# Kernel optimization log

Measured on AMD Instinct MI355X. Metric: run time of the kernel, lower is better.

The kernel has to match this reference:

```python
import jax, jax.numpy as jnp
import numpy as np

N_NODES = 100000
N_EDGES = 1600000


def setup_inputs() -> dict:
    key = jax.random.key(0)
    ks = jax.random.split(key, 6)
    x = jax.random.normal(ks[0], (N_NODES, 128), dtype=jnp.float32)
    edge_index = jax.random.randint(ks[1], (2, N_EDGES), 0, N_NODES, dtype=jnp.int64)
    # glorot-ish scaled weights
    W0 = jax.random.normal(ks[2], (128, 64), dtype=jnp.float32) * (1.0 / np.sqrt(128))
    W1 = jax.random.normal(ks[3], (64, 64), dtype=jnp.float32) * (1.0 / np.sqrt(64))
    W2 = jax.random.normal(ks[4], (64, 40), dtype=jnp.float32) * (1.0 / np.sqrt(64))
    b0 = jnp.zeros((64,), jnp.float32)
    b1 = jnp.zeros((64,), jnp.float32)
    b2 = jnp.zeros((40,), jnp.float32)
    return {"x": x, "edge_index": edge_index, "W0": W0, "b0": b0,
            "W1": W1, "b1": b1, "W2": W2, "b2": b2}


def _gcn_norm(edge_index, n, dtype):
    # PyG gcn_norm: add self-loops, deg over targets, norm = d^-1/2[src]*d^-1/2[dst]
    loop = jnp.arange(n, dtype=edge_index.dtype)
    src = jnp.concatenate([edge_index[0], loop])
    dst = jnp.concatenate([edge_index[1], loop])
    deg = jax.ops.segment_sum(jnp.ones_like(dst, dtype=dtype), dst, num_segments=n)
    dinv = jnp.where(deg > 0, jax.lax.rsqrt(deg), 0.0)
    return src, dst, dinv[src] * dinv[dst]


def reference(x, edge_index, W0, b0, W1, b1, W2, b2):
    n = x.shape[0]
    src, dst, norm = _gcn_norm(edge_index, n, x.dtype)

    def conv(h, W, b):
        h = h @ W                                   # [N, out]
        msg = h[src] * norm[:, None]                # gather + per-edge scale
        return jax.ops.segment_sum(msg, dst, num_segments=n) + b

    # dropout skipped (eval mode); relu between layers per forward()
    h = jax.nn.relu(conv(x, W0, b0))
    h = jax.nn.relu(conv(h, W1, b1))
    return conv(h, W2, b2)
```

## Files before the change

### kernel.cpp

```cpp
#include <hip/hip_runtime.h>
#include <hip/hip_fp16.h>


#define ALIGN256(x) (((size_t)(x) + 255) & ~(size_t)255)

typedef _Float16 f16;
typedef f16 f16x8 __attribute__((ext_vector_type(8)));
typedef float f32x4 __attribute__((ext_vector_type(4)));


__global__ __launch_bounds__(256) void k_coarse(const int* __restrict__ ei,
                                                int* __restrict__ ccnt,
                                                int E, int NBUK) {
    __shared__ int h[512];
    int t = threadIdx.x;
    for (int i = t; i < NBUK; i += 256) h[i] = 0;
    __syncthreads();
    int e0 = blockIdx.x * 8192;
    int e1 = min(e0 + 8192, E);
    for (int e = e0 + t; e < e1; e += 256) atomicAdd(&h[ei[E + e] >> 8], 1);
    __syncthreads();
    for (int i = t; i < NBUK; i += 256) {
        int c = h[i];
        if (c) atomicAdd(&ccnt[i], c);
    }
}


__global__ __launch_bounds__(256) void k_cscan(const int* __restrict__ ccnt,
                                               int* __restrict__ cbase,
                                               int* __restrict__ cpos,
                                               int* __restrict__ row_start,
                                               int NBUK, int E, int N) {
    __shared__ int sd[256];
    int t = threadIdx.x;
    int i0 = 2 * t, i1 = 2 * t + 1;
    int v0 = (i0 < NBUK) ? ccnt[i0] : 0;
    int v1 = (i1 < NBUK) ? ccnt[i1] : 0;
    int s = v0 + v1;
    sd[t] = s;
    __syncthreads();
    for (int off = 1; off < 256; off <<= 1) {
        int u = (t >= off) ? sd[t - off] : 0;
        __syncthreads();
        sd[t] += u;
        __syncthreads();
    }
    int base = sd[t] - s;
    if (i0 < NBUK) { cbase[i0] = base;      cpos[i0] = base; }
    if (i1 < NBUK) { cbase[i1] = base + v0; cpos[i1] = base + v0; }
    if (t == 0) { cbase[NBUK] = E; row_start[N] = E; }
}


__global__ __launch_bounds__(256) void k_passA(const int* __restrict__ ei,
                                               int* __restrict__ cpos,
                                               unsigned int* __restrict__ stage,
                                               int E, int NBUK) {
    __shared__ int h[512];
    __shared__ int base[512];
    int t = threadIdx.x;
    for (int i = t; i < NBUK; i += 256) h[i] = 0;
    __syncthreads();
    int e0 = blockIdx.x * 8192;
    int e1 = min(e0 + 8192, E);
    for (int e = e0 + t; e < e1; e += 256) atomicAdd(&h[ei[E + e] >> 8], 1);
    __syncthreads();
    for (int b = t; b < NBUK; b += 256) {
        int c = h[b];
        base[b] = c ? atomicAdd(&cpos[b], c) : 0;
        h[b] = 0;
    }
    __syncthreads();
    for (int e = e0 + t; e < e1; e += 256) {
        unsigned int s = (unsigned int)ei[e];
        int d = ei[E + e];
        int b = d >> 8;
        int off = base[b] + atomicAdd(&h[b], 1);
        stage[off] = ((unsigned int)(d & 255) << 24) | s;
    }
}


__global__ __launch_bounds__(256) void k_B1(const unsigned int* __restrict__ stage,
                                            const int* __restrict__ cbase,
                                            int* __restrict__ row_start,
                                            float* __restrict__ dinv, int N) {
    __shared__ int cnt[256];
    __shared__ int sd[256];
    int b = blockIdx.x;
    int n0 = b << 8;
    int t = threadIdx.x;
    cnt[t] = 0;
    __syncthreads();
    int s0 = cbase[b], s1 = cbase[b + 1];
    for (int j = s0 + t; j < s1; j += 256) atomicAdd(&cnt[stage[j] >> 24], 1);
    __syncthreads();
    int c = cnt[t];
    sd[t] = c;
    __syncthreads();
    for (int off = 1; off < 256; off <<= 1) {
        int u = (t >= off) ? sd[t - off] : 0;
        __syncthreads();
        sd[t] += u;
        __syncthreads();
    }
    int excl = sd[t] - c;
    int node = n0 + t;
    if (node < N) {
        row_start[node] = s0 + excl;
        dinv[node] = 1.0f / sqrtf((float)(c + 1));
    }
}


__global__ __launch_bounds__(256) void k_B2(const unsigned int* __restrict__ stage,
                                            const int* __restrict__ cbase,
                                            const int* __restrict__ row_start,
                                            const float* __restrict__ dinv,
                                            int2* __restrict__ ep, int N) {
    __shared__ int lpos[256];
    __shared__ float ld[256];
    int b = blockIdx.x;
    int n0 = b << 8;
    int t = threadIdx.x;
    int node = n0 + t;
    if (node < N) {
        lpos[t] = row_start[node];
        ld[t] = dinv[node];
    }
    __syncthreads();
    int s0 = cbase[b], s1 = cbase[b + 1];
    for (int j = s0 + t; j < s1; j += 256) {
        unsigned int v = stage[j];
        int li = v >> 24;
        int src = v & 0xFFFFFF;
        int slot = atomicAdd(&lpos[li], 1);
        ep[slot] = make_int2(src, __float_as_int(dinv[src] * ld[li]));
    }
}


template <int K, int OUT, int NF, typename XT>
__global__ __launch_bounds__(256) void k_mgemm(const XT* __restrict__ X,
                                               const float* __restrict__ W,
                                               __half* __restrict__ Y, int N) {
    constexpr int NC = NF * 16;
    constexpr int NT = K / 32;
    __shared__ f16 Wl[NT * NF * 4 * 128];

    int tid = threadIdx.x;
    for (int idx = tid; idx < K * NC; idx += 256) {
        int k = idx / NC;
        int n = idx - k * NC;
        float v = (n < OUT) ? W[k * OUT + n] : 0.0f;
        int t = k >> 5, h = (k >> 3) & 3, j = k & 7, f = n >> 4, nn = n & 15;
        Wl[((t * NF + f) * 4 + h) * 128 + nn * 8 + j] = (f16)v;
    }
    __syncthreads();

    int lane = tid & 63;
    int wid = tid >> 6;
    int h = lane >> 4;
    int nn = lane & 15;
    int row = blockIdx.x * 64 + (wid << 4) + nn;
    bool valid = row < N;

    f32x4 acc[NF];
#pragma unroll
    for (int f = 0; f < NF; ++f) acc[f] = (f32x4){0.f, 0.f, 0.f, 0.f};

#pragma unroll
    for (int t = 0; t < NT; ++t) {
        f16x8 xf;
        if (valid) {
            if constexpr (sizeof(XT) == 4) {
                const float* xp = (const float*)X + (size_t)row * K + (t << 5) + (h << 3);
                float4 u0 = *(const float4*)xp;
                float4 u1 = *(const float4*)(xp + 4);
                xf[0] = (f16)u0.x; xf[1] = (f16)u0.y; xf[2] = (f16)u0.z; xf[3] = (f16)u0.w;
                xf[4] = (f16)u1.x; xf[5] = (f16)u1.y; xf[6] = (f16)u1.z; xf[7] = (f16)u1.w;
            } else {
                xf = *(const f16x8*)((const __half*)X + (size_t)row * K + (t << 5) + (h << 3));
            }
        } else {
#pragma unroll
            for (int j = 0; j < 8; ++j) xf[j] = (f16)0.f;
        }
#pragma unroll
        for (int f = 0; f < NF; ++f) {
            f16x8 wf = *(const f16x8*)&Wl[((t * NF + f) * 4 + h) * 128 + nn * 8];
            acc[f] = __builtin_amdgcn_mfma_f32_16x16x32_f16(wf, xf, acc[f], 0, 0, 0);
        }
    }

    if (valid) {
#pragma unroll
        for (int f = 0; f < NF; ++f) {
            int c = (f << 4) + (h << 2);
            if (c < OUT) {
                __half2 p0 = __floats2half2_rn(acc[f][0], acc[f][1]);
                __half2 p1 = __floats2half2_rn(acc[f][2], acc[f][3]);
                uint2 pk = make_uint2(*(unsigned int*)&p0, *(unsigned int*)&p1);
                *(uint2*)&Y[(size_t)row * OUT + c] = pk;
            }
        }
    }
}


__device__ __forceinline__ void fma8(float4& a0, float4& a1, uint4 hv, float w) {
    __half2* hp = (__half2*)&hv;
    float2 f0 = __half22float2(hp[0]);
    float2 f1 = __half22float2(hp[1]);
    float2 f2 = __half22float2(hp[2]);
    float2 f3 = __half22float2(hp[3]);
    a0.x += f0.x * w; a0.y += f0.y * w; a0.z += f1.x * w; a0.w += f1.y * w;
    a1.x += f2.x * w; a1.y += f2.y * w; a1.z += f3.x * w; a1.w += f3.y * w;
}

template <int NV, int F, int RELU, typename OutT>
__global__ __launch_bounds__(256) void k_agg(const __half* __restrict__ H,
                                             const int* __restrict__ row_start,
                                             const int2* __restrict__ ep,
                                             const float* __restrict__ dinv,
                                             const float* __restrict__ bias,
                                             OutT* __restrict__ out, int N) {
    int tid = threadIdx.x;
    int lane = tid & 63;
    int sub = lane >> 3;
    int lq = lane & 7;
    int node = blockIdx.x * 32 + (tid >> 6) * 8 + sub;
    if (node >= N) return;
    const bool act = (NV == 8) || (lq < NV);

    int jb = row_start[node];
    int je = row_start[node + 1];
    float dv = dinv[node];

    float4 a0 = make_float4(0.f, 0.f, 0.f, 0.f);
    float4 a1 = make_float4(0.f, 0.f, 0.f, 0.f);
    if (act) {
        uint4 hv = *(const uint4*)&H[(size_t)node * F + 8 * lq];
        fma8(a0, a1, hv, dv * dv);
    }

    int j = jb;
    for (; j + 8 <= je; j += 8) {
        int2 e0 = ep[j],     e1 = ep[j + 1], e2 = ep[j + 2], e3 = ep[j + 3];
        int2 e4 = ep[j + 4], e5 = ep[j + 5], e6 = ep[j + 6], e7 = ep[j + 7];
        if (act) {
            uint4 h0 = *(const uint4*)&H[(size_t)e0.x * F + 8 * lq];
            uint4 h1 = *(const uint4*)&H[(size_t)e1.x * F + 8 * lq];
            uint4 h2 = *(const uint4*)&H[(size_t)e2.x * F + 8 * lq];
            uint4 h3 = *(const uint4*)&H[(size_t)e3.x * F + 8 * lq];
            uint4 h4 = *(const uint4*)&H[(size_t)e4.x * F + 8 * lq];
            uint4 h5 = *(const uint4*)&H[(size_t)e5.x * F + 8 * lq];
            uint4 h6 = *(const uint4*)&H[(size_t)e6.x * F + 8 * lq];
            uint4 h7 = *(const uint4*)&H[(size_t)e7.x * F + 8 * lq];
            fma8(a0, a1, h0, __int_as_float(e0.y));
            fma8(a0, a1, h1, __int_as_float(e1.y));
            fma8(a0, a1, h2, __int_as_float(e2.y));
            fma8(a0, a1, h3, __int_as_float(e3.y));
            fma8(a0, a1, h4, __int_as_float(e4.y));
            fma8(a0, a1, h5, __int_as_float(e5.y));
            fma8(a0, a1, h6, __int_as_float(e6.y));
            fma8(a0, a1, h7, __int_as_float(e7.y));
        }
    }
    for (; j + 2 <= je; j += 2) {
        int2 e0 = ep[j], e1 = ep[j + 1];
        if (act) {
            uint4 h0 = *(const uint4*)&H[(size_t)e0.x * F + 8 * lq];
            uint4 h1 = *(const uint4*)&H[(size_t)e1.x * F + 8 * lq];
            fma8(a0, a1, h0, __int_as_float(e0.y));
            fma8(a0, a1, h1, __int_as_float(e1.y));
        }
    }
    if (j < je) {
        int2 e = ep[j];
        if (act) {
            uint4 h = *(const uint4*)&H[(size_t)e.x * F + 8 * lq];
            fma8(a0, a1, h, __int_as_float(e.y));
        }
    }

    if (act) {
        float4 b0 = *(const float4*)&bias[8 * lq];
        float4 b1 = *(const float4*)&bias[8 * lq + 4];
        a0.x += b0.x; a0.y += b0.y; a0.z += b0.z; a0.w += b0.w;
        a1.x += b1.x; a1.y += b1.y; a1.z += b1.z; a1.w += b1.w;
        if (RELU) {
            a0.x = fmaxf(a0.x, 0.f); a0.y = fmaxf(a0.y, 0.f);
            a0.z = fmaxf(a0.z, 0.f); a0.w = fmaxf(a0.w, 0.f);
            a1.x = fmaxf(a1.x, 0.f); a1.y = fmaxf(a1.y, 0.f);
            a1.z = fmaxf(a1.z, 0.f); a1.w = fmaxf(a1.w, 0.f);
        }
        if constexpr (sizeof(OutT) == 2) {
            __half2 p0 = __floats2half2_rn(a0.x, a0.y);
            __half2 p1 = __floats2half2_rn(a0.z, a0.w);
            __half2 p2 = __floats2half2_rn(a1.x, a1.y);
            __half2 p3 = __floats2half2_rn(a1.z, a1.w);
            uint4 pk = make_uint4(*(unsigned int*)&p0, *(unsigned int*)&p1,
                                  *(unsigned int*)&p2, *(unsigned int*)&p3);
            *(uint4*)&out[(size_t)node * F + 8 * lq] = pk;
        } else {
            *(float4*)&out[(size_t)node * F + 8 * lq] = a0;
            *(float4*)&out[(size_t)node * F + 8 * lq + 4] = a1;
        }
    }
}


extern "C" void kernel_launch(void* const* d_in, const int* in_sizes, int n_in,
                              void* d_out, int out_size, void* d_ws, size_t ws_size,
                              hipStream_t stream) {
    const float* x  = (const float*)d_in[0];
    const int*   ei = (const int*)d_in[1];
    const float* W0 = (const float*)d_in[2];
    const float* b0 = (const float*)d_in[3];
    const float* W1 = (const float*)d_in[4];
    const float* b1 = (const float*)d_in[5];
    const float* W2 = (const float*)d_in[6];
    const float* b2 = (const float*)d_in[7];
    float* out = (float*)d_out;

    const int N = in_sizes[0] / 128;
    const int E = in_sizes[1] / 2;
    const int NBUK = (N + 255) >> 8;

    char* w = (char*)d_ws;
    size_t off = 0;
    int*    ccnt      = (int*)(w + off);    off = ALIGN256(off + (size_t)NBUK * 4);
    int*    cbase     = (int*)(w + off);    off = ALIGN256(off + (size_t)(NBUK + 1) * 4);
    int*    cpos      = (int*)(w + off);    off = ALIGN256(off + (size_t)NBUK * 4);
    int*    row_start = (int*)(w + off);    off = ALIGN256(off + (size_t)(N + 1) * 4);
    float*  dinv      = (float*)(w + off);  off = ALIGN256(off + (size_t)N * 4);
    int2*   ep        = (int2*)(w + off);   off = ALIGN256(off + (size_t)E * 8);
    __half* bufH      = (__half*)(w + off); off = ALIGN256(off + (size_t)N * 64 * 2);
    __half* bufG      = (__half*)(w + off); off = ALIGN256(off + (size_t)N * 64 * 2);
    unsigned int* stage = (unsigned int*)bufG;

    const int gGemm = (N + 63) / 64;
    const int gAgg  = (N + 31) / 32;
    const int gPA   = (E + 8191) / 8192;

    hipMemsetAsync(ccnt, 0, (size_t)NBUK * 4, stream);
    k_mgemm<128, 64, 4><<<gGemm, 256, 0, stream>>>(x, W0, bufH, N);
    k_coarse<<<gPA, 256, 0, stream>>>(ei, ccnt, E, NBUK);
    k_cscan<<<1, 256, 0, stream>>>(ccnt, cbase, cpos, row_start, NBUK, E, N);
    k_passA<<<gPA, 256, 0, stream>>>(ei, cpos, stage, E, NBUK);
    k_B1<<<NBUK, 256, 0, stream>>>(stage, cbase, row_start, dinv, N);
    k_B2<<<NBUK, 256, 0, stream>>>(stage, cbase, row_start, dinv, ep, N);

    k_agg<8, 64, 1, __half><<<gAgg, 256, 0, stream>>>(bufH, row_start, ep, dinv, b0, bufG, N);
    k_mgemm<64, 64, 4><<<gGemm, 256, 0, stream>>>(bufG, W1, bufH, N);
    k_agg<8, 64, 1, __half><<<gAgg, 256, 0, stream>>>(bufH, row_start, ep, dinv, b1, bufG, N);
    k_mgemm<64, 40, 3><<<gGemm, 256, 0, stream>>>(bufG, W2, bufH, N);
    k_agg<5, 40, 0, float><<<gAgg, 256, 0, stream>>>(bufH, row_start, ep, dinv, b2, out, N);
}
```

Baseline: 304.8 us.

## Sort nodes by degree for aggregation and fuse scans into last-block epilogues

Builds a degree histogram in k_B1 and a degree-sorted node permutation in a new k_perm kernel. The three aggregation kernels process nodes in that order, so the 8-lane groups in a wavefront handle nodes of similar degree and lose less time to divergence. The separate coarse scan launch is folded into k_coarse through a last-block-done counter, which removes one launch. The cost is an extra kernel, an indirect perm read per node, and scattered row_start, H and output accesses because neighbouring lanes no longer work on neighbouring node ids.

```diff
diff --git a/kernel.cpp b/kernel.cpp
--- a/kernel.cpp
+++ b/kernel.cpp
@@ -11,8 +11,13 @@
 
 __global__ __launch_bounds__(256) void k_coarse(const int* __restrict__ ei,
                                                 int* __restrict__ ccnt,
-                                                int E, int NBUK) {
+                                                int* __restrict__ done,
+                                                int* __restrict__ cbase,
+                                                int* __restrict__ cpos,
+                                                int* __restrict__ row_start,
+                                                int E, int N, int NBUK, int nblk) {
     __shared__ int h[512];
+    __shared__ int lastblk;
     int t = threadIdx.x;
     for (int i = t; i < NBUK; i += 256) h[i] = 0;
     __syncthreads();
@@ -24,16 +29,12 @@
         int c = h[i];
         if (c) atomicAdd(&ccnt[i], c);
     }
-}
-
-
-__global__ __launch_bounds__(256) void k_cscan(const int* __restrict__ ccnt,
-                                               int* __restrict__ cbase,
-                                               int* __restrict__ cpos,
-                                               int* __restrict__ row_start,
-                                               int NBUK, int E, int N) {
+    __threadfence();
+    if (t == 0) lastblk = (atomicAdd(done, 1) == nblk - 1) ? 1 : 0;
+    __syncthreads();
+    if (!lastblk) return;
+
     __shared__ int sd[256];
-    int t = threadIdx.x;
     int i0 = 2 * t, i1 = 2 * t + 1;
     int v0 = (i0 < NBUK) ? ccnt[i0] : 0;
     int v1 = (i1 < NBUK) ? ccnt[i1] : 0;
@@ -85,9 +86,15 @@
 __global__ __launch_bounds__(256) void k_B1(const unsigned int* __restrict__ stage,
                                             const int* __restrict__ cbase,
                                             int* __restrict__ row_start,
-                                            float* __restrict__ dinv, int N) {
+                                            float* __restrict__ dinv,
+                                            int* __restrict__ dhist,
+                                            int* __restrict__ done2,
+                                            int* __restrict__ dbase,
+                                            int* __restrict__ dpos,
+                                            int N, int nblk) {
     __shared__ int cnt[256];
     __shared__ int sd[256];
+    __shared__ int lastblk;
     int b = blockIdx.x;
     int n0 = b << 8;
     int t = threadIdx.x;
@@ -110,7 +117,24 @@
     if (node < N) {
         row_start[node] = s0 + excl;
         dinv[node] = 1.0f / sqrtf((float)(c + 1));
-    }
+        atomicAdd(&dhist[min(c, 255)], 1);
+    }
+    __threadfence();
+    if (t == 0) lastblk = (atomicAdd(done2, 1) == nblk - 1) ? 1 : 0;
+    __syncthreads();
+    if (!lastblk) return;
+
+    int v = dhist[t];
+    sd[t] = v;
+    __syncthreads();
+    for (int off = 1; off < 256; off <<= 1) {
+        int u = (t >= off) ? sd[t - off] : 0;
+        __syncthreads();
+        sd[t] += u;
+        __syncthreads();
+    }
+    dbase[t] = sd[t] - v;
+    dpos[t]  = sd[t] - v;
 }
 
 
@@ -137,6 +161,32 @@
         int src = v & 0xFFFFFF;
         int slot = atomicAdd(&lpos[li], 1);
         ep[slot] = make_int2(src, __float_as_int(dinv[src] * ld[li]));
+    }
+}
+
+
+__global__ __launch_bounds__(256) void k_perm(const int* __restrict__ row_start,
+                                              int* __restrict__ dpos,
+                                              int* __restrict__ perm, int N) {
+    __shared__ int h[256];
+    __shared__ int base[256];
+    int t = threadIdx.x;
+    h[t] = 0;
+    __syncthreads();
+    int node = blockIdx.x * 256 + t;
+    int deg = 0;
+    if (node < N) {
+        deg = min(row_start[node + 1] - row_start[node], 255);
+        atomicAdd(&h[deg], 1);
+    }
+    __syncthreads();
+    int c = h[t];
+    base[t] = c ? atomicAdd(&dpos[t], c) : 0;
+    h[t] = 0;
+    __syncthreads();
+    if (node < N) {
+        int slot = base[deg] + atomicAdd(&h[deg], 1);
+        perm[slot] = node;
     }
 }
 
@@ -225,13 +275,15 @@
                                              const int2* __restrict__ ep,
                                              const float* __restrict__ dinv,
                                              const float* __restrict__ bias,
+                                             const int* __restrict__ perm,
                                              OutT* __restrict__ out, int N) {
     int tid = threadIdx.x;
     int lane = tid & 63;
     int sub = lane >> 3;
     int lq = lane & 7;
-    int node = blockIdx.x * 32 + (tid >> 6) * 8 + sub;
-    if (node >= N) return;
+    int idx = blockIdx.x * 32 + (tid >> 6) * 8 + sub;
+    if (idx >= N) return;
+    int node = perm[idx];
     const bool act = (NV == 8) || (lq < NV);
 
     int jb = row_start[node];
@@ -331,11 +383,17 @@
 
     char* w = (char*)d_ws;
     size_t off = 0;
-    int*    ccnt      = (int*)(w + off);    off = ALIGN256(off + (size_t)NBUK * 4);
+    int*    ccnt      = (int*)(w + off);    off = ALIGN256(off + (size_t)(NBUK + 2 + 256) * 4);
+    int*    done      = ccnt + NBUK;
+    int*    done2     = ccnt + NBUK + 1;
+    int*    dhist     = ccnt + NBUK + 2;
     int*    cbase     = (int*)(w + off);    off = ALIGN256(off + (size_t)(NBUK + 1) * 4);
     int*    cpos      = (int*)(w + off);    off = ALIGN256(off + (size_t)NBUK * 4);
+    int*    dbase     = (int*)(w + off);    off = ALIGN256(off + (size_t)256 * 4);
+    int*    dpos      = (int*)(w + off);    off = ALIGN256(off + (size_t)256 * 4);
     int*    row_start = (int*)(w + off);    off = ALIGN256(off + (size_t)(N + 1) * 4);
     float*  dinv      = (float*)(w + off);  off = ALIGN256(off + (size_t)N * 4);
+    int*    perm      = (int*)(w + off);    off = ALIGN256(off + (size_t)N * 4);
     int2*   ep        = (int2*)(w + off);   off = ALIGN256(off + (size_t)E * 8);
     __half* bufH      = (__half*)(w + off); off = ALIGN256(off + (size_t)N * 64 * 2);
     __half* bufG      = (__half*)(w + off); off = ALIGN256(off + (size_t)N * 64 * 2);
@@ -344,18 +402,19 @@
     const int gGemm = (N + 63) / 64;
     const int gAgg  = (N + 31) / 32;
     const int gPA   = (E + 8191) / 8192;
-
-    hipMemsetAsync(ccnt, 0, (size_t)NBUK * 4, stream);
+    const int gPerm = (N + 255) / 256;
+
+    hipMemsetAsync(ccnt, 0, (size_t)(NBUK + 2 + 256) * 4, stream);
     k_mgemm<128, 64, 4><<<gGemm, 256, 0, stream>>>(x, W0, bufH, N);
-    k_coarse<<<gPA, 256, 0, stream>>>(ei, ccnt, E, NBUK);
-    k_cscan<<<1, 256, 0, stream>>>(ccnt, cbase, cpos, row_start, NBUK, E, N);
+    k_coarse<<<gPA, 256, 0, stream>>>(ei, ccnt, done, cbase, cpos, row_start, E, N, NBUK, gPA);
     k_passA<<<gPA, 256, 0, stream>>>(ei, cpos, stage, E, NBUK);
-    k_B1<<<NBUK, 256, 0, stream>>>(stage, cbase, row_start, dinv, N);
+    k_B1<<<NBUK, 256, 0, stream>>>(stage, cbase, row_start, dinv, dhist, done2, dbase, dpos, N, NBUK);
     k_B2<<<NBUK, 256, 0, stream>>>(stage, cbase, row_start, dinv, ep, N);
-
-    k_agg<8, 64, 1, __half><<<gAgg, 256, 0, stream>>>(bufH, row_start, ep, dinv, b0, bufG, N);
+    k_perm<<<gPerm, 256, 0, stream>>>(row_start, dpos, perm, N);
+
+    k_agg<8, 64, 1, __half><<<gAgg, 256, 0, stream>>>(bufH, row_start, ep, dinv, b0, perm, bufG, N);
     k_mgemm<64, 64, 4><<<gGemm, 256, 0, stream>>>(bufG, W1, bufH, N);
-    k_agg<8, 64, 1, __half><<<gAgg, 256, 0, stream>>>(bufH, row_start, ep, dinv, b1, bufG, N);
+    k_agg<8, 64, 1, __half><<<gAgg, 256, 0, stream>>>(bufH, row_start, ep, dinv, b1, perm, bufG, N);
     k_mgemm<64, 40, 3><<<gGemm, 256, 0, stream>>>(bufG, W2, bufH, N);
-    k_agg<5, 40, 0, float><<<gAgg, 256, 0, stream>>>(bufH, row_start, ep, dinv, b2, out, N);
-}
+    k_agg<5, 40, 0, float><<<gAgg, 256, 0, stream>>>(bufH, row_start, ep, dinv, b2, perm, out, N);
+}
```

After: 616.1 us. +102.1%, slower.
